# Optimization experiments

Measured on AMD Instinct MI355X. Metric: run time of the kernel, lower is better.

## Reference

```python
import jax, jax.numpy as jnp
import numpy as np

N_EMBD = 768
N_HEAD = 12
HEAD_DIM = N_EMBD // N_HEAD


def setup_inputs() -> dict:
    key = jax.random.key(0)
    k1, k2, k3 = jax.random.split(key, 3)
    x = jax.random.normal(k1, (2, 2048, N_EMBD), dtype=jnp.float32)
    # Dense kernels (no bias), scaled like Glorot-ish init
    w_qkv = jax.random.normal(k2, (N_EMBD, 3 * N_EMBD), dtype=jnp.float32) * (1.0 / np.sqrt(N_EMBD))
    w_proj = jax.random.normal(k3, (N_EMBD, N_EMBD), dtype=jnp.float32) * (1.0 / np.sqrt(N_EMBD))
    return {"x": x, "w_qkv": w_qkv, "w_proj": w_proj}


def reference(x, w_qkv, w_proj):
    b, t, _ = x.shape
    qkv = x @ w_qkv                                  # [b, t, 3*n_embd]
    q, k, v = jnp.split(qkv, 3, axis=-1)
    def split_heads(z):
        return z.reshape(b, t, N_HEAD, HEAD_DIM).transpose(0, 2, 1, 3)  # [b, h, t, d]
    q, k, v = split_heads(q), split_heads(k), split_heads(v)
    scale = jnp.float32(HEAD_DIM) ** -0.5
    att = jnp.einsum('bhqd,bhkd->bhqk', q, k) * scale  # [b, h, t, t]
    # lower-triangular causal mask, additive -1e9 on masked (future) positions
    mask = jnp.tril(jnp.ones((t, t), dtype=jnp.float32))
    att = att + (1.0 - mask)[None, None, :, :] * jnp.float32(-1e9)
    att = jax.nn.softmax(att, axis=-1)
    out = jnp.einsum('bhqk,bhkd->bhqd', att, v)      # [b, h, t, d]
    out = out.transpose(0, 2, 1, 3).reshape(b, t, N_EMBD)
    return out @ w_proj
```

## Files before the change

kernel.cpp:

```cpp
#include <hip/hip_runtime.h>

#define T_SEQ   2048
#define EMBD    768
#define N_HEAD  12
#define HDIM    64
#define BATCH   2

typedef float f32x4 __attribute__((ext_vector_type(4)));
typedef short bf16x8 __attribute__((ext_vector_type(8)));
typedef unsigned short u16;
typedef unsigned int u32;
typedef u16 u16x4 __attribute__((ext_vector_type(4)));

#define MFMA_BF16(a, b, c) __builtin_amdgcn_mfma_f32_16x16x32_bf16((a), (b), (c), 0, 0, 0)

__device__ __forceinline__ u16 f2bf(float f) {
    union { float f; unsigned u; } v; v.f = f;
    unsigned r = v.u + 0x7fffu + ((v.u >> 16) & 1u);
    return (u16)(r >> 16);
}

__device__ __forceinline__ u32 pack2(float hi, float lo) {
    union { float f; u32 u; } a, b;
    a.f = hi; b.f = lo;
    return __builtin_amdgcn_perm(a.u, b.u, 0x07060302u);
}

__device__ __forceinline__ void gload_lds16(const u16* g, u16* l) {
    __builtin_amdgcn_global_load_lds(
        (const __attribute__((address_space(1))) u32*)g,
        (__attribute__((address_space(3))) u32*)l, 16, 0, 0);
}

__global__ __launch_bounds__(256) void prep_kernel(
    const float* __restrict__ x, const float* __restrict__ wq,
    const float* __restrict__ wp, u16* __restrict__ xb,
    u16* __restrict__ wqT, u16* __restrict__ wpT)
{
    const int bid = blockIdx.x;
    const int tid = threadIdx.x;
    if (bid < 1536) {
        const int i = bid * 2048 + tid * 8;
        const float4 f0 = *(const float4*)&x[i];
        const float4 f1 = *(const float4*)&x[i + 4];
        bf16x8 r;
        r[0] = (short)f2bf(f0.x); r[1] = (short)f2bf(f0.y);
        r[2] = (short)f2bf(f0.z); r[3] = (short)f2bf(f0.w);
        r[4] = (short)f2bf(f1.x); r[5] = (short)f2bf(f1.y);
        r[6] = (short)f2bf(f1.z); r[7] = (short)f2bf(f1.w);
        *(bf16x8*)&xb[i] = r;
        return;
    }
    __shared__ float tile[32][33];
    const float* W; u16* Wt; int N, t;
    if (bid < 3264) { W = wq; Wt = wqT; N = 2304; t = bid - 1536; }
    else            { W = wp; Wt = wpT; N = 768;  t = bid - 3264; }
    const int ntiles = N / 32;
    const int n0 = (t % ntiles) * 32;
    const int k0 = (t / ntiles) * 32;
    const int c  = tid & 31;
    const int r8 = tid >> 5;
#pragma unroll
    for (int rr = r8; rr < 32; rr += 8)
        tile[rr][c] = W[(size_t)(k0 + rr) * N + n0 + c];
    __syncthreads();
#pragma unroll
    for (int rr = r8; rr < 32; rr += 8)
        Wt[(size_t)(n0 + rr) * 768 + k0 + c] = f2bf(tile[c][rr]);
}

template <int NCOLS, int SCATTER, int TM>
__global__ __launch_bounds__(256, 3) void mfma_gemm(
    const u16* __restrict__ A, const u16* __restrict__ Bt,
    float* __restrict__ C, u16* __restrict__ Qo, u16* __restrict__ Ko,
    u16* __restrict__ Vo)
{
    constexpr int MT = TM / 32;
    constexpr int AI = TM / 32;
    __shared__ u16 As[TM * 64];
    __shared__ u16 Bs[128 * 64];
    const int tid  = threadIdx.x;
    const int lane = tid & 63, wave = tid >> 6;
    const int l15  = lane & 15, quad = lane >> 4;
    const int wy   = wave >> 1, wx = wave & 1;
    const int row0 = blockIdx.y * TM, col0 = blockIdx.x * 128;

    const int sr = lane >> 3;
    const int sc = lane & 7;
    const int g  = sc ^ sr;
    const u16* gA[AI]; const u16* gB[4]; u16* lA[AI]; u16* lB[4];
#pragma unroll
    for (int i = 0; i < AI; ++i) {
        const int rb = (i * 4 + wave) * 8;
        gA[i] = &A[(size_t)(row0 + rb + sr) * 768 + g * 8];
        lA[i] = &As[rb * 64];
    }
#pragma unroll
    for (int i = 0; i < 4; ++i) {
        const int rb = (i * 4 + wave) * 8;
        gB[i] = &Bt[(size_t)(col0 + rb + sr) * 768 + g * 8];
        lB[i] = &Bs[rb * 64];
    }

    f32x4 acc[MT][4];
#pragma unroll
    for (int i = 0; i < MT; ++i)
#pragma unroll
        for (int j = 0; j < 4; ++j) acc[i][j] = (f32x4){0.f, 0.f, 0.f, 0.f};

    for (int k0 = 0; k0 < 768; k0 += 64) {
        __syncthreads();
#pragma unroll
        for (int i = 0; i < AI; ++i) gload_lds16(gA[i] + k0, lA[i]);
#pragma unroll
        for (int i = 0; i < 4; ++i) gload_lds16(gB[i] + k0, lB[i]);
        __syncthreads();
#pragma unroll
        for (int ks = 0; ks < 2; ++ks) {
            bf16x8 af[MT], bfr[4];
#pragma unroll
            for (int mt = 0; mt < MT; ++mt)
                af[mt] = *(const bf16x8*)&As[(wy * (TM / 2) + mt * 16 + l15) * 64 +
                                             (((ks * 4 + quad) ^ (l15 & 7)) * 8)];
#pragma unroll
            for (int nt = 0; nt < 4; ++nt)
                bfr[nt] = *(const bf16x8*)&Bs[(wx * 64 + nt * 16 + l15) * 64 +
                                              (((ks * 4 + quad) ^ (l15 & 7)) * 8)];
#pragma unroll
            for (int mt = 0; mt < MT; ++mt)
#pragma unroll
                for (int nt = 0; nt < 4; ++nt)
                    acc[mt][nt] = MFMA_BF16(af[mt], bfr[nt], acc[mt][nt]);
        }
    }

    const float qscale = 0.18033688f;
#pragma unroll
    for (int mt = 0; mt < MT; ++mt) {
#pragma unroll
        for (int nt = 0; nt < 4; ++nt) {
            const int col = col0 + wx * 64 + nt * 16 + l15;
            if (SCATTER) {
                const int which = col / 768;
                const int hh = (col - which * 768) >> 6;
                const int dd = col & 63;
                if (which == 2) {
                    const int row = row0 + wy * (TM / 2) + mt * 16 + quad * 4;
                    const int bb = row >> 11, t0 = row & 2047;
                    u16x4 pk;
#pragma unroll
                    for (int r = 0; r < 4; ++r) pk[r] = f2bf(acc[mt][nt][r]);
                    *(u16x4*)&Vo[((size_t)(bb * N_HEAD + hh) * HDIM + dd) * T_SEQ + t0] = pk;
                } else {
                    u16* dst = (which == 0) ? Qo : Ko;
                    const float sc2 = (which == 0) ? qscale : 1.0f;
                    const size_t hb = (size_t)hh * T_SEQ * HDIM + dd;
#pragma unroll
                    for (int r = 0; r < 4; ++r) {
                        const int row = row0 + wy * (TM / 2) + mt * 16 + quad * 4 + r;
                        const int bb = row >> 11, tt = row & 2047;
                        dst[(size_t)bb * N_HEAD * T_SEQ * HDIM + hb + (size_t)tt * HDIM] =
                            f2bf(acc[mt][nt][r] * sc2);
                    }
                }
            } else {
#pragma unroll
                for (int r = 0; r < 4; ++r) {
                    const int row = row0 + wy * (TM / 2) + mt * 16 + quad * 4 + r;
                    C[(size_t)row * NCOLS + col] = acc[mt][nt][r];
                }
            }
        }
    }
}

__global__ __launch_bounds__(256, 3) void attn_mfma(
    const u16* __restrict__ Q, const u16* __restrict__ K,
    const u16* __restrict__ Vt, u16* __restrict__ Aout)
{
    __shared__ float Comb[5120];
    u16* PsAll = (u16*)Comb;

    const int tid  = threadIdx.x;
    const int lane = tid & 63, wave = tid >> 6;
    const int l15  = lane & 15, quad = lane >> 4;

    const int f    = blockIdx.x;
    const int slot = f >> 3;
    const int bh   = (f & 7) * 3 + (slot >> 5);
    const int p    = slot & 31;
    const int b    = bh / N_HEAD, h = bh - b * N_HEAD;

    const int j      = (wave < 2) ? (63 - p) : p;
    const int parity = wave & 1;
    const int qb     = j * 32;
    const int nk     = (j >> 1) + 1;
    const size_t base = (size_t)bh * T_SEQ * HDIM;

    bf16x8 qf[2][2];
#pragma unroll
    for (int jq = 0; jq < 2; ++jq)
#pragma unroll
        for (int ks = 0; ks < 2; ++ks)
            qf[jq][ks] = *(const bf16x8*)&Q[base + (size_t)(qb + jq * 16 + l15) * HDIM +
                                            ks * 32 + quad * 8];

    f32x4 o[2][4], l_acc[2];
#pragma unroll
    for (int jq = 0; jq < 2; ++jq) {
        l_acc[jq] = (f32x4){0.f, 0.f, 0.f, 0.f};
#pragma unroll
        for (int nt = 0; nt < 4; ++nt) o[jq][nt] = (f32x4){0.f, 0.f, 0.f, 0.f};
    }

    bf16x8 onesf;
#pragma unroll
    for (int u = 0; u < 8; ++u) onesf[u] = (short)0x3F80;

    u16* myPs = PsAll + wave * 2304;

    bf16x8 kc[4][2];
    {
        const int k0 = parity * 64;
#pragma unroll
        for (int i = 0; i < 4; ++i)
#pragma unroll
            for (int ks = 0; ks < 2; ++ks)
                kc[i][ks] = *(const bf16x8*)&K[base + (size_t)(k0 + i * 16 + l15) * HDIM +
                                               ks * 32 + quad * 8];
    }

    for (int kt = parity; kt < nk; kt += 2) {
        const int k0 = kt * 64;
        const bool pf = (kt + 2 < nk);

        f32x4 s[4][2];
#pragma unroll
        for (int i = 0; i < 4; ++i)
#pragma unroll
            for (int jq = 0; jq < 2; ++jq) s[i][jq] = (f32x4){0.f, 0.f, 0.f, 0.f};
#pragma unroll
        for (int ks = 0; ks < 2; ++ks)
#pragma unroll
            for (int i = 0; i < 2; ++i)
#pragma unroll
                for (int jq = 0; jq < 2; ++jq)
                    s[i][jq] = MFMA_BF16(kc[i][ks], qf[jq][ks], s[i][jq]);

        bf16x8 vf0[4];
#pragma unroll
        for (int nt = 0; nt < 4; ++nt)
            vf0[nt] = *(const bf16x8*)&Vt[base + (size_t)(nt * 16 + l15) * T_SEQ +
                                          k0 + quad * 8];

#pragma unroll
        for (int i = 0; i < 2; ++i)
#pragma unroll
            for (int jq = 0; jq < 2; ++jq) {
                float pv[4];
                if (k0 + i * 16 + 15 > qb + jq * 16) {
                    const int q = qb + jq * 16 + l15;
#pragma unroll
                    for (int r = 0; r < 4; ++r) {
                        const int key = k0 + i * 16 + quad * 4 + r;
                        pv[r] = exp2f((key > q) ? -1e30f : s[i][jq][r]);
                    }
                } else {
#pragma unroll
                    for (int r = 0; r < 4; ++r) pv[r] = exp2f(s[i][jq][r]);
                }
                uint2 w;
                w.x = pack2(pv[1], pv[0]);
                w.y = pack2(pv[3], pv[2]);
                *(uint2*)&myPs[(jq * 16 + l15) * 72 + i * 16 + quad * 4] = w;
            }

#pragma unroll
        for (int ks = 0; ks < 2; ++ks)
#pragma unroll
            for (int i = 2; i < 4; ++i)
#pragma unroll
                for (int jq = 0; jq < 2; ++jq)
                    s[i][jq] = MFMA_BF16(kc[i][ks], qf[jq][ks], s[i][jq]);

        if (pf) {
            const int kn0 = k0 + 128;
#pragma unroll
            for (int i = 0; i < 4; ++i)
#pragma unroll
                for (int ks = 0; ks < 2; ++ks)
                    kc[i][ks] = *(const bf16x8*)&K[base +
                        (size_t)(kn0 + i * 16 + l15) * HDIM + ks * 32 + quad * 8];
        }

        bf16x8 pa0[2];
#pragma unroll
        for (int jq = 0; jq < 2; ++jq)
            pa0[jq] = *(const bf16x8*)&myPs[(jq * 16 + l15) * 72 + quad * 8];

#pragma unroll
        for (int i = 2; i < 4; ++i)
#pragma unroll
            for (int jq = 0; jq < 2; ++jq) {
                float pv[4];
                if (k0 + i * 16 + 15 > qb + jq * 16) {
                    const int q = qb + jq * 16 + l15;
#pragma unroll
                    for (int r = 0; r < 4; ++r) {
                        const int key = k0 + i * 16 + quad * 4 + r;
                        pv[r] = exp2f((key > q) ? -1e30f : s[i][jq][r]);
                    }
                } else {
#pragma unroll
                    for (int r = 0; r < 4; ++r) pv[r] = exp2f(s[i][jq][r]);
                }
                uint2 w;
                w.x = pack2(pv[1], pv[0]);
                w.y = pack2(pv[3], pv[2]);
                *(uint2*)&myPs[(jq * 16 + l15) * 72 + i * 16 + quad * 4] = w;
            }

#pragma unroll
        for (int jq = 0; jq < 2; ++jq) {
#pragma unroll
            for (int nt = 0; nt < 4; ++nt)
                o[jq][nt] = MFMA_BF16(pa0[jq], vf0[nt], o[jq][nt]);
            l_acc[jq] = MFMA_BF16(pa0[jq], onesf, l_acc[jq]);
        }

        bf16x8 vf1[4];
#pragma unroll
        for (int nt = 0; nt < 4; ++nt)
            vf1[nt] = *(const bf16x8*)&Vt[base + (size_t)(nt * 16 + l15) * T_SEQ +
                                          k0 + 32 + quad * 8];
        bf16x8 pa1[2];
#pragma unroll
        for (int jq = 0; jq < 2; ++jq)
            pa1[jq] = *(const bf16x8*)&myPs[(jq * 16 + l15) * 72 + 32 + quad * 8];
#pragma unroll
        for (int jq = 0; jq < 2; ++jq) {
#pragma unroll
            for (int nt = 0; nt < 4; ++nt)
                o[jq][nt] = MFMA_BF16(pa1[jq], vf1[nt], o[jq][nt]);
            l_acc[jq] = MFMA_BF16(pa1[jq], onesf, l_acc[jq]);
        }
    }

    __syncthreads();
    if (parity == 1) {
        float* R = Comb + (wave >> 1) * 2560;
#pragma unroll
        for (int jq = 0; jq < 2; ++jq) {
#pragma unroll
            for (int nt = 0; nt < 4; ++nt)
#pragma unroll
                for (int r = 0; r < 4; ++r)
                    R[(jq * 16 + nt * 4 + r) * 64 + lane] = o[jq][nt][r];
#pragma unroll
            for (int r = 0; r < 4; ++r)
                R[(32 + jq * 4 + r) * 64 + lane] = l_acc[jq][r];
        }
    }
    __syncthreads();
    if (parity == 0) {
        const float* R = Comb + (wave >> 1) * 2560;
#pragma unroll
        for (int jq = 0; jq < 2; ++jq) {
#pragma unroll
            for (int nt = 0; nt < 4; ++nt)
#pragma unroll
                for (int r = 0; r < 4; ++r)
                    o[jq][nt][r] += R[(jq * 16 + nt * 4 + r) * 64 + lane];
#pragma unroll
            for (int r = 0; r < 4; ++r)
                l_acc[jq][r] += R[(32 + jq * 4 + r) * 64 + lane];
        }
#pragma unroll
        for (int jq = 0; jq < 2; ++jq) {
            f32x4 inv;
#pragma unroll
            for (int r = 0; r < 4; ++r) inv[r] = 1.0f / l_acc[jq][r];
#pragma unroll
            for (int nt = 0; nt < 4; ++nt) {
                const int d = nt * 16 + l15;
#pragma unroll
                for (int r = 0; r < 4; ++r) {
                    const int q = qb + jq * 16 + quad * 4 + r;
                    Aout[(size_t)(b * T_SEQ + q) * EMBD + h * HDIM + d] =
                        f2bf(o[jq][nt][r] * inv[r]);
                }
            }
        }
    }
}

extern "C" void kernel_launch(void* const* d_in, const int* in_sizes, int n_in,
                              void* d_out, int out_size, void* d_ws, size_t ws_size,
                              hipStream_t stream)
{
    (void)in_sizes; (void)n_in; (void)out_size; (void)ws_size;
    const float* x      = (const float*)d_in[0];
    const float* w_qkv  = (const float*)d_in[1];
    const float* w_proj = (const float*)d_in[2];
    float* out = (float*)d_out;

    u16* ws = (u16*)d_ws;
    const size_t NX  = (size_t)BATCH * T_SEQ * EMBD;
    const size_t NWQ = (size_t)EMBD * 3 * EMBD;
    const size_t NWP = (size_t)EMBD * EMBD;
    const size_t SZ  = (size_t)BATCH * N_HEAD * T_SEQ * HDIM;
    u16* xb     = ws;
    u16* wqkvT  = xb + NX;
    u16* wprojT = wqkvT + NWQ;
    u16* Qb     = wprojT + NWP;
    u16* Kb     = Qb + SZ;
    u16* Vtb    = Kb + SZ;
    u16* Ab     = Vtb + SZ;

    dim3 blk(256);
    prep_kernel<<<dim3(3840), blk, 0, stream>>>(x, w_qkv, w_proj, xb, wqkvT, wprojT);

    mfma_gemm<3 * EMBD, 1, 128><<<dim3(3 * EMBD / 128, BATCH * T_SEQ / 128), blk, 0, stream>>>(
        xb, wqkvT, nullptr, Qb, Kb, Vtb);

    attn_mfma<<<dim3(32 * N_HEAD * BATCH), blk, 0, stream>>>(Qb, Kb, Vtb, Ab);

    mfma_gemm<EMBD, 0, 64><<<dim3(EMBD / 128, BATCH * T_SEQ / 64), blk, 0, stream>>>(
        Ab, wprojT, out, nullptr, nullptr, nullptr);
}
```

Baseline: 164.4 us.

## Rotate wave-to-work mapping per block and drop cross-iteration K prefetch

After: 158.4 us. 1.04x faster.

```diff
diff --git a/kernel.cpp b/kernel.cpp
--- a/kernel.cpp
+++ b/kernel.cpp
@@ -191,8 +191,9 @@
     const int p    = slot & 31;
     const int b    = bh / N_HEAD, h = bh - b * N_HEAD;
 
-    const int j      = (wave < 2) ? (63 - p) : p;
-    const int parity = wave & 1;
+    const int wsel   = (wave + f) & 3;
+    const int j      = (wsel < 2) ? (63 - p) : p;
+    const int parity = wsel & 1;
     const int qb     = j * 32;
     const int nk     = (j >> 1) + 1;
     const size_t base = (size_t)bh * T_SEQ * HDIM;
@@ -219,20 +220,8 @@
 
     u16* myPs = PsAll + wave * 2304;
 
-    bf16x8 kc[4][2];
-    {
-        const int k0 = parity * 64;
-#pragma unroll
-        for (int i = 0; i < 4; ++i)
-#pragma unroll
-            for (int ks = 0; ks < 2; ++ks)
-                kc[i][ks] = *(const bf16x8*)&K[base + (size_t)(k0 + i * 16 + l15) * HDIM +
-                                               ks * 32 + quad * 8];
-    }
-
     for (int kt = parity; kt < nk; kt += 2) {
         const int k0 = kt * 64;
-        const bool pf = (kt + 2 < nk);
 
         f32x4 s[4][2];
 #pragma unroll
@@ -240,18 +229,26 @@
 #pragma unroll
             for (int jq = 0; jq < 2; ++jq) s[i][jq] = (f32x4){0.f, 0.f, 0.f, 0.f};
 #pragma unroll
-        for (int ks = 0; ks < 2; ++ks)
-#pragma unroll
-            for (int i = 0; i < 2; ++i)
+        for (int ks = 0; ks < 2; ++ks) {
+            bf16x8 kf[4];
+#pragma unroll
+            for (int i = 0; i < 4; ++i)
+                kf[i] = *(const bf16x8*)&K[base + (size_t)(k0 + i * 16 + l15) * HDIM +
+                                           ks * 32 + quad * 8];
+#pragma unroll
+            for (int i = 0; i < 4; ++i)
 #pragma unroll
                 for (int jq = 0; jq < 2; ++jq)
-                    s[i][jq] = MFMA_BF16(kc[i][ks], qf[jq][ks], s[i][jq]);
-
-        bf16x8 vf0[4];
+                    s[i][jq] = MFMA_BF16(kf[i], qf[jq][ks], s[i][jq]);
+        }
+
+        bf16x8 vf[4][2];
 #pragma unroll
         for (int nt = 0; nt < 4; ++nt)
-            vf0[nt] = *(const bf16x8*)&Vt[base + (size_t)(nt * 16 + l15) * T_SEQ +
-                                          k0 + quad * 8];
+#pragma unroll
+            for (int ks = 0; ks < 2; ++ks)
+                vf[nt][ks] = *(const bf16x8*)&Vt[base + (size_t)(nt * 16 + l15) * T_SEQ +
+                                                 k0 + ks * 32 + quad * 8];
 
 #pragma unroll
         for (int i = 0; i < 2; ++i)
@@ -275,24 +272,6 @@
                 *(uint2*)&myPs[(jq * 16 + l15) * 72 + i * 16 + quad * 4] = w;
             }
 
-#pragma unroll
-        for (int ks = 0; ks < 2; ++ks)
-#pragma unroll
-            for (int i = 2; i < 4; ++i)
-#pragma unroll
-                for (int jq = 0; jq < 2; ++jq)
-                    s[i][jq] = MFMA_BF16(kc[i][ks], qf[jq][ks], s[i][jq]);
-
-        if (pf) {
-            const int kn0 = k0 + 128;
-#pragma unroll
-            for (int i = 0; i < 4; ++i)
-#pragma unroll
-                for (int ks = 0; ks < 2; ++ks)
-                    kc[i][ks] = *(const bf16x8*)&K[base +
-                        (size_t)(kn0 + i * 16 + l15) * HDIM + ks * 32 + quad * 8];
-        }
-
         bf16x8 pa0[2];
 #pragma unroll
         for (int jq = 0; jq < 2; ++jq)
@@ -324,15 +303,10 @@
         for (int jq = 0; jq < 2; ++jq) {
 #pragma unroll
             for (int nt = 0; nt < 4; ++nt)
-                o[jq][nt] = MFMA_BF16(pa0[jq], vf0[nt], o[jq][nt]);
+                o[jq][nt] = MFMA_BF16(pa0[jq], vf[nt][0], o[jq][nt]);
             l_acc[jq] = MFMA_BF16(pa0[jq], onesf, l_acc[jq]);
         }
 
-        bf16x8 vf1[4];
-#pragma unroll
-        for (int nt = 0; nt < 4; ++nt)
-            vf1[nt] = *(const bf16x8*)&Vt[base + (size_t)(nt * 16 + l15) * T_SEQ +
-                                          k0 + 32 + quad * 8];
         bf16x8 pa1[2];
 #pragma unroll
         for (int jq = 0; jq < 2; ++jq)
@@ -341,14 +315,14 @@
         for (int jq = 0; jq < 2; ++jq) {
 #pragma unroll
             for (int nt = 0; nt < 4; ++nt)
-                o[jq][nt] = MFMA_BF16(pa1[jq], vf1[nt], o[jq][nt]);
+                o[jq][nt] = MFMA_BF16(pa1[jq], vf[nt][1], o[jq][nt]);
             l_acc[jq] = MFMA_BF16(pa1[jq], onesf, l_acc[jq]);
         }
     }
 
     __syncthreads();
     if (parity == 1) {
-        float* R = Comb + (wave >> 1) * 2560;
+        float* R = Comb + (wsel >> 1) * 2560;
 #pragma unroll
         for (int jq = 0; jq < 2; ++jq) {
 #pragma unroll
@@ -363,7 +337,7 @@
     }
     __syncthreads();
     if (parity == 0) {
-        const float* R = Comb + (wave >> 1) * 2560;
+        const float* R = Comb + (wsel >> 1) * 2560;
 #pragma unroll
         for (int jq = 0; jq < 2; ++jq) {
 #pragma unroll
```
